# Kernel tuning notes

Hardware: AMD Instinct MI355X
Metric: run time of the kernel (lower is better)

## Reference

```python
import jax, jax.numpy as jnp
import numpy as np

B, N, K, C_IN, D = 4, 2048, 16, 480, 64
EPS = 1e-5


def _c1(x, w, b):
    # 1x1 Conv1d: x (B,C,N), w (O,C) -> (B,O,N)
    return jnp.einsum('oc,bcn->bon', w, x) + b[:, None]


def _c2(x, w, b):
    # 1x1 Conv2d: x (B,C,J,N), w (O,C) -> (B,O,J,N)
    return jnp.einsum('oc,bcjn->bojn', w, x) + b[:, None, None]


def _bn(x, g, b):
    # eval-mode BatchNorm2d with running_mean=0, running_var=1
    return x * (g / jnp.sqrt(1.0 + EPS))[:, None, None] + b[:, None, None]


def _mlp_res(x, w1, b1, w2, b2, ws, bs):
    return _c1(jax.nn.relu(_c1(x, w1, b1)), w2, b2) + _c1(x, ws, bs)


def _group(f, idx):
    # f (B,C,N), idx (B,K,N) int -> out[b,c,j,n] = f[b,c,idx[b,j,n]]  -> (B,C,K,N)
    return jax.vmap(lambda ff, ii: ff[:, ii])(f, idx)


def _knn_idx(xyz):
    # xyz (B,3,N) -> idx (B,K,N), excluding the self point (nearest neighbor)
    pts = xyz.transpose(0, 2, 1)  # (B,N,3)
    sq = jnp.sum(pts * pts, -1)
    d2 = sq[:, :, None] + sq[:, None, :] - 2.0 * jnp.einsum('bnd,bmd->bnm', pts, pts)
    _, idx = jax.lax.top_k(-d2, K + 1)  # (B,N,K+1), nearest first
    return idx.transpose(0, 2, 1)[:, 1:, :]  # drop self -> (B,K,N)


def _forward(idx, feature, xyz, bt1_w, bt1_b, bt2_w, bt2_b, bts_w, bts_b,
             q_w, q_b, k_w, k_b, v_w, v_b,
             fd1_w, fd1_b, fd_g, fd_bb, fd2_w, fd2_b,
             fg1_w, fg1_b, fg_g, fg_bb, fg2_w, fg2_b,
             at_w, at_b, m41_w, m41_b, m42_w, m42_b):
    x = _mlp_res(feature, bt1_w, bt1_b, bt2_w, bt2_b, bts_w, bts_b)  # (B,64,N)
    q = _c1(x, q_w, q_b)
    k = _c1(x, k_w, k_b)
    v = _c1(x, v_w, v_b)

    group_xyz = _group(xyz, idx)                       # (B,3,K,N)
    rel_xyz = xyz[:, :, None, :] - group_xyz           # (B,3,K,N)
    pos_enc = _c2(jax.nn.relu(_bn(_c2(rel_xyz, fd1_w, fd1_b), fd_g, fd_bb)), fd2_w, fd2_b)  # (B,64,K,N)

    k_local = _group(k, idx)                           # (B,64,K,N)
    v_local = _group(v, idx)
    qk_rel = q[:, :, None, :] - k_local
    attn = _c2(jax.nn.relu(_bn(_c2(qk_rel + pos_enc, fg1_w, fg1_b), fg_g, fg_bb)), fg2_w, fg2_b)  # (B,64,K,N)

    attn1 = attn.transpose(0, 1, 3, 2)                 # (B,64,N,K)
    # ConvTranspose2d(64,64,(4,1),(4,1)) with kernel==stride: out[b,o,4n+r,f] = sum_c x[b,c,n,f]*W[c,o,r] + bias[o]
    y = jnp.einsum('bcnf,cor->bonrf', attn1, at_w)
    y = y.reshape(y.shape[0], y.shape[1], -1, y.shape[4]) + at_b[None, :, None, None]  # (B,64,4N,K)
    attn = jax.nn.softmax(y, axis=1)

    value_rel = (v_local + pos_enc).transpose(0, 1, 3, 2)   # (B,64,N,K)
    value = jnp.repeat(value_rel, 4, axis=2)                # nearest upsample (4,1) -> (B,64,4N,K)

    res = jnp.einsum('bmnf,bmnf->bmn', attn, value)         # (B,64,4N)
    identity = jnp.repeat(x, 4, axis=2)                     # nearest upsample x4 -> (B,64,4N)
    res = res + identity
    completion = _c1(jax.nn.relu(_c1(res, m41_w, m41_b)), m42_w, m42_b)  # (B,3,4N)
    return completion, res


def setup_inputs() -> dict:
    key = jax.random.key(0)
    ks = jax.random.split(key, 24)
    i = iter(range(24))

    def w(shape):
        return (jax.random.normal(ks[next(i)], shape, dtype=jnp.float32) * 0.05)

    z = lambda n: jnp.zeros((n,), jnp.float32)
    o = lambda n: jnp.ones((n,), jnp.float32)
    return {
        'feature': jax.random.normal(ks[next(i)], (B, C_IN, N), dtype=jnp.float32),
        'xyz': jax.random.normal(ks[next(i)], (B, 3, N), dtype=jnp.float32),
        'bt1_w': w((D, C_IN)), 'bt1_b': z(D),
        'bt2_w': w((D, D)), 'bt2_b': z(D),
        'bts_w': w((D, C_IN)), 'bts_b': z(D),
        'q_w': w((D, D)), 'q_b': z(D),
        'k_w': w((D, D)), 'k_b': z(D),
        'v_w': w((D, D)), 'v_b': z(D),
        'fd1_w': w((D, 3)), 'fd1_b': z(D), 'fd_g': o(D), 'fd_bb': z(D),
        'fd2_w': w((D, D)), 'fd2_b': z(D),
        'fg1_w': w((4 * D, D)), 'fg1_b': z(4 * D), 'fg_g': o(4 * D), 'fg_bb': z(4 * D),
        'fg2_w': w((D, 4 * D)), 'fg2_b': z(D),
        'at_w': w((D, D, 4)), 'at_b': z(D),
        'm41_w': w((D, D)), 'm41_b': z(D),
        'm42_w': w((3, D)), 'm42_b': z(3),
    }


def reference(feature, xyz, bt1_w, bt1_b, bt2_w, bt2_b, bts_w, bts_b,
              q_w, q_b, k_w, k_b, v_w, v_b,
              fd1_w, fd1_b, fd_g, fd_bb, fd2_w, fd2_b,
              fg1_w, fg1_b, fg_g, fg_bb, fg2_w, fg2_b,
              at_w, at_b, m41_w, m41_b, m42_w, m42_b):
    idx = _knn_idx(xyz)
    return _forward(idx, feature, xyz, bt1_w, bt1_b, bt2_w, bt2_b, bts_w, bts_b,
                    q_w, q_b, k_w, k_b, v_w, v_b,
                    fd1_w, fd1_b, fd_g, fd_bb, fd2_w, fd2_b,
                    fg1_w, fg1_b, fg_g, fg_bb, fg2_w, fg2_b,
                    at_w, at_b, m41_w, m41_b, m42_w, m42_b)
```

## Files before the change

kernel.cpp:

```cpp
#include <hip/hip_runtime.h>

#define B_ 4
#define N_ 2048
#define K_ 16
#define CIN_ 480
#define UPN_ 8192
#define M_ (B_*N_*K_)
#define MX_ (B_*N_)
#define KCAP 448

#define KNN_BLK 2048
#define TR_BLK  1920
#define PREP_BLK 1047

typedef unsigned int u32;
typedef unsigned short u16;
typedef unsigned long long u64;
typedef __attribute__((ext_vector_type(8))) short short8;
typedef __attribute__((ext_vector_type(4))) float f32x4;

#define DEV static __device__ __forceinline__

DEV float b2f(u16 h){ return __uint_as_float(((u32)h)<<16); }
DEV u16 f2b(float f){
  u32 u = __float_as_uint(f);
  u32 r = u + 0x7fffu + ((u>>16)&1u);
  return (u16)(r>>16);
}
DEV u32 cvtpk(float a, float b){
  u32 r; asm("v_cvt_pk_bf16_f32 %0, %1, %2" : "=v"(r) : "v"(a), "v"(b));
  return r;
}
DEV u64 cvtpk4(float a, float b, float c, float d){
  return (u64)cvtpk(a,b) | ((u64)cvtpk(c,d)<<32);
}
DEV bool detect_bf(const void* fg){ return ((((const u32*)fg)[0]) & 0xFFFFu) == 0x3F80u; }
DEV float ld(const void* p, int i, bool bf){
  return bf ? b2f(((const u16*)p)[i]) : ((const float*)p)[i];
}
DEV u64 makekey(float d2, int m){
  u32 bits = __float_as_uint(d2);
  bits = (bits & 0x80000000u) ? ~bits : (bits | 0x80000000u);
  return ((u64)bits<<32) | (u32)m;
}
DEV int swz64 (int row, int colByte){ return row*128 + (colByte ^ ((row&7)<<4)); }
DEV int swz128(int row, int colByte){ return row*256 + (colByte ^ ((row&7)<<4)); }

__global__ __launch_bounds__(256) void setup_kernel(
    const void* __restrict__ feature, const void* __restrict__ xyz,
    const void* __restrict__ bt1_w, const void* __restrict__ bt1_b,
    const void* __restrict__ bt2_w, const void* __restrict__ bt2_b,
    const void* __restrict__ bts_w, const void* __restrict__ bts_b,
    const void* __restrict__ q_w, const void* __restrict__ q_b,
    const void* __restrict__ k_w, const void* __restrict__ k_b,
    const void* __restrict__ v_w, const void* __restrict__ v_b,
    const void* __restrict__ fd1_w, const void* __restrict__ fd1_b,
    const void* __restrict__ fd_g, const void* __restrict__ fd_bb,
    const void* __restrict__ fd2_w, const void* __restrict__ fd2_b,
    const void* __restrict__ fg1_w, const void* __restrict__ fg1_b,
    const void* __restrict__ fg_g, const void* __restrict__ fg_bb,
    const void* __restrict__ fg2_w, const void* __restrict__ fg2_b,
    const void* __restrict__ at_w, const void* __restrict__ at_b,
    const void* __restrict__ m41_w, const void* __restrict__ m41_b,
    const void* __restrict__ m42_w, const void* __restrict__ m42_b,
    float* __restrict__ W, u16* __restrict__ WB,
    u16* __restrict__ fxbT, float* __restrict__ fxyz, int* __restrict__ idx)
{
  __shared__ alignas(16) unsigned char smem[50208];
  int blkid = blockIdx.x;
  bool bf = detect_bf(fd_g);

  if(blkid < KNN_BLK){
    float* px = (float*)smem;
    float* py = px + N_;
    float* pz = py + N_;
    float* sq = pz + N_;
    u64*  sbuf = (u64*)(sq + N_);
    u64*  smin = sbuf + 4*KCAP;
    int*  scnt = (int*)(smin + 256);
    u64*  stau = (u64*)(scnt + 256);
    int bx = blkid & 511;
    int b = blkid >> 9;
    int base = b*3*N_;
    bool w0 = (bx==0);
    for(int i=threadIdx.x;i<N_;i+=256){
      float xx=ld(xyz,base+i,bf), yy=ld(xyz,base+N_+i,bf), zz=ld(xyz,base+2*N_+i,bf);
      px[i]=xx; py[i]=yy; pz[i]=zz; sq[i]=xx*xx+yy*yy+zz*zz;
      if(w0){ fxyz[base+i]=xx; fxyz[base+N_+i]=yy; fxyz[base+2*N_+i]=zz; }
    }
    __syncthreads();
    int w = threadIdx.x>>6, l = threadIdx.x&63;
    int q = bx*4 + w;
    float qx=px[q], qy=py[q], qz=pz[q], qs=sq[q];
    float d2c[32];
    u64 best=~0ull;
    #pragma unroll
    for(int j=0;j<32;j++){
      int m = l*32 + ((j+l)&31);
      float d2 = (qs+sq[m]) - 2.0f*(qx*px[m]+qy*py[m]+qz*pz[m]);
      d2c[j]=d2;
      u64 key = makekey(d2, m);
      best = key<best ? key : best;
    }
    smin[w*64+l]=best;
    __syncthreads();
    {
      int rank=0;
      for(int i=0;i<64;i++) rank += (smin[w*64+i] < best);
      if(rank==16) stau[w] = best;
    }
    __syncthreads();
    u64 tau = stau[w];
    int myc=0;
    #pragma unroll
    for(int j=0;j<32;j++){
      int m = l*32 + ((j+l)&31);
      myc += (makekey(d2c[j], m) <= tau);
    }
    scnt[w*64+l]=myc;
    __syncthreads();
    int off=0, tot=0;
    for(int i=0;i<64;i++){
      int c = scnt[w*64+i];
      tot += c;
      off += (i<l) ? c : 0;
    }
    #pragma unroll
    for(int j=0;j<32;j++){
      int m = l*32 + ((j+l)&31);
      u64 key = makekey(d2c[j], m);
      if(key<=tau && off<KCAP){ sbuf[w*KCAP+off]=key; off++; }
    }
    __syncthreads();
    if(tot>KCAP) tot=KCAP;
    for(int p=l; p<tot; p+=64){
      u64 kk = sbuf[w*KCAP+p];
      int rk=0;
      for(int i=0;i<tot;i++) rk += (sbuf[w*KCAP+i] < kk);
      if(rk>=1 && rk<17) idx[(b*K_+(rk-1))*N_+q] = ((int)(kk & 0xffffffffu)) & (N_-1);
    }
    return;
  }

  if(blkid < KNN_BLK + TR_BLK){
    u16 (*s)[34] = (u16(*)[34])smem;
    int t = blkid - KNN_BLK;
    int ntile = t & 31;  int rest = t >> 5;
    int ctile = rest % 15; int b = rest / 15;
    int tx = threadIdx.x & 31, ty = threadIdx.x >> 5;
    u64 base = (u64)b*CIN_*N_;
    #pragma unroll
    for(int r=0;r<4;r++){
      int c = ctile*32 + ty + r*8;
      u64 i = base + (u64)c*N_ + ntile*64 + tx*2;
      u32 v;
      if(bf) v = *(const u32*)((const u16*)feature + i);
      else {
        float a0=((const float*)feature)[i], a1=((const float*)feature)[i+1];
        v = (u32)f2b(a0) | ((u32)f2b(a1)<<16);
      }
      s[tx*2  ][ty + r*8] = (u16)v;
      s[tx*2+1][ty + r*8] = (u16)(v>>16);
    }
    __syncthreads();
    #pragma unroll
    for(int r=0;r<4;r++){
      int i2 = r*256 + threadIdx.x;
      int nrow = i2 >> 4, cp = i2 & 15;
      u32 v = *(const u32*)&s[nrow][cp*2];
      int n = ntile*64 + nrow;
      *(u32*)(fxbT + (u64)b*N_*CIN_ + (u64)n*CIN_ + ctile*32 + cp*2) = v;
    }
    return;
  }

  int t = (blkid - (KNN_BLK + TR_BLK))*256 + threadIdx.x;
  const float inv = 0.9999950000374997f;
  if(t < 30720) return; t -= 30720;
  if(t < 30720) return; t -= 30720;
  if(t < 4096) return; t -= 4096;
  if(t < 4096) return; t -= 4096;
  if(t < 4096) return; t -= 4096;
  if(t < 4096) return; t -= 4096;
  if(t < 256){
    int o=t>>2, j=t&3; float s = ld(fd_g,o,bf)*inv;
    W[77824+t] = (j<3) ? s*ld(fd1_w,o*3+j,bf) : (s*ld(fd1_b,o,bf) + ld(fd_bb,o,bf));
    return;
  } t -= 256;
  if(t < 4096) return; t -= 4096;
  if(t < 16384) return; t -= 16384;
  if(t < 256){ float s=ld(fg_g,t,bf)*inv; W[98560+t] = s*ld(fg1_b,t,bf) + ld(fg_bb,t,bf); return; } t -= 256;
  if(t < 16384) return; t -= 16384;
  if(t < 16384) return; t -= 16384;
  if(t < 4096){ int m=t>>6, o=t&63; W[131584+t] = ld(m41_w,o*64+m,bf); return; } t -= 4096;
  if(t < 192){ W[135680+t] = ld(m42_w,t,bf); return; } t -= 192;
  if(t < 64){ W[135872+t] = ld(bt1_b,t,bf); return; } t -= 64;
  if(t < 64){ W[135936+t] = ld(bts_b,t,bf); return; } t -= 64;
  if(t < 64){ W[136000+t] = ld(bt2_b,t,bf); return; } t -= 64;
  if(t < 64){ W[136064+t] = ld(q_b,t,bf); return; } t -= 64;
  if(t < 64){ W[136128+t] = ld(k_b,t,bf); return; } t -= 64;
  if(t < 64){ W[136192+t] = ld(v_b,t,bf); return; } t -= 64;
  if(t < 64){ W[136256+t] = ld(fd2_b,t,bf); return; } t -= 64;
  if(t < 64){ W[136320+t] = ld(fg2_b,t,bf); return; } t -= 64;
  if(t < 64){ W[136384+t] = ld(at_b,t,bf); return; } t -= 64;
  if(t < 64){ W[136448+t] = ld(m41_b,t,bf); return; } t -= 64;
  if(t < 3){ W[136512+t] = ld(m42_b,t,bf); return; } t -= 3;
  if(t < 16384){ int o=t>>6; float s=ld(fg_g,o,bf)*inv; WB[t] = f2b(s*ld(fg1_w,t,bf)); return; } t -= 16384;
  if(t < 16384){ WB[16384+t] = f2b(ld(fg2_w,t,bf)); return; } t -= 16384;
  if(t < 16384){ int j=t>>6, c=t&63;
                 WB[32768+t] = f2b(ld(at_w,(c*64+(j&63))*4+(j>>6),bf)); return; } t -= 16384;
  if(t < 256){ W[136576+t] = ld(at_b,t&63,bf); return; } t -= 256;
  if(t < 4096){ WB[49152+t] = f2b(ld(fd2_w,t,bf)); return; } t -= 4096;
  if(t < 30720){ WB[53248+t] = f2b(ld(bt1_w,t,bf)); return; } t -= 30720;
  if(t < 30720){ WB[83968+t] = f2b(ld(bts_w,t,bf)); return; } t -= 30720;
  if(t < 4096){ WB[114688+t] = f2b(ld(bt2_w,t,bf)); return; } t -= 4096;
  if(t < 4096){ WB[118784+t] = f2b(ld(q_w,t,bf)); return; } t -= 4096;
  if(t < 4096){ WB[122880+t] = f2b(ld(k_w,t,bf)); return; } t -= 4096;
  if(t < 4096){ WB[126976+t] = f2b(ld(v_w,t,bf)); return; }
}

__global__ __launch_bounds__(256) void gemm480_mfma(const u16* __restrict__ A,
    const u16* __restrict__ Wt, const float* __restrict__ bias,
    u16* __restrict__ hout, float* __restrict__ xsout)
{
  int tid=threadIdx.x, w=tid>>6, lane=tid&63;
  int rbase=(blockIdx.x*4+w)*16;
  int cbase=blockIdx.y*64;
  int lr=lane&15, lk=(lane>>4)*8;
  f32x4 acc[4];
  #pragma unroll
  for(int j=0;j<4;j++) acc[j]=(f32x4){0.f,0.f,0.f,0.f};
  for(int kc=0;kc<CIN_;kc+=32){
    short8 a = *(const short8*)(A + (u64)(rbase+lr)*CIN_ + kc + lk);
    #pragma unroll
    for(int tj=0;tj<4;tj++){
      short8 bb = *(const short8*)(Wt + (u64)(cbase+tj*16+lr)*CIN_ + kc + lk);
      acc[tj] = __builtin_amdgcn_mfma_f32_16x16x32_bf16(a, bb, acc[tj], 0,0,0);
    }
  }
  int rq=(lane>>4)*4;
  #pragma unroll
  for(int tj=0;tj<4;tj++){
    int col = cbase + tj*16 + lr;
    float bv = bias[col];
    #pragma unroll
    for(int reg=0;reg<4;reg++){
      u64 row = rbase + rq + reg;
      float vv = acc[tj][reg] + bv;
      if(blockIdx.y==0) hout[row*64 + col] = f2b(fmaxf(vv,0.f));
      else              xsout[row*64 + (col-64)] = vv;
    }
  }
}

__global__ __launch_bounds__(256) void xqkv_mfma(const u16* __restrict__ A,
    const u16* __restrict__ Wbt2, const float* __restrict__ bbt2,
    const float* __restrict__ xs,
    const u16* __restrict__ Wqkv, const float* __restrict__ bqkv,
    float* __restrict__ x, float* __restrict__ qkvout)
{
  __shared__ alignas(16) unsigned char lds[8192];
  int tid=threadIdx.x, w=tid>>6, lane=tid&63;
  int lr=lane&15, lk=(lane>>4)*8, rq=(lane>>4)*4;
  unsigned char* Lw = lds + w*2048;
  u64 rbase=(u64)(blockIdx.x*4+w)*16;

  {
    f32x4 ax[4];
    #pragma unroll
    for(int i=0;i<4;i++) ax[i]=(f32x4){0.f,0.f,0.f,0.f};
    #pragma unroll
    for(int kc=0;kc<64;kc+=32){
      short8 hf = *(const short8*)(A + (rbase+lr)*64 + kc + lk);
      #pragma unroll
      for(int t=0;t<4;t++){
        short8 wf = *(const short8*)(Wbt2 + (u64)(t*16+lr)*64 + kc + lk);
        ax[t] = __builtin_amdgcn_mfma_f32_16x16x32_bf16(wf, hf, ax[t], 0,0,0);
      }
    }
    #pragma unroll
    for(int t=0;t<4;t++){
      f32x4 bb = *(const f32x4*)(bbt2 + t*16 + rq);
      f32x4 sv = *(const f32x4*)(xs + (rbase+lr)*64 + t*16 + rq);
      f32x4 xv;
      #pragma unroll
      for(int reg=0;reg<4;reg++) xv[reg] = ax[t][reg] + bb[reg] + sv[reg];
      *(f32x4*)(x + (rbase+lr)*64 + t*16 + rq) = xv;
      *(u64*)(Lw + swz64(lr, (t*16+rq)*2)) = cvtpk4(xv[0],xv[1],xv[2],xv[3]);
    }
  }
  __syncthreads();
  #pragma unroll
  for(int g=0;g<3;g++){
    f32x4 aq[4];
    #pragma unroll
    for(int i=0;i<4;i++) aq[i]=(f32x4){0.f,0.f,0.f,0.f};
    #pragma unroll
    for(int kc=0;kc<64;kc+=32){
      short8 hf = *(const short8*)(Lw + swz64(lr, (kc+lk)*2));
      #pragma unroll
      for(int t=0;t<4;t++){
        short8 wf = *(const short8*)(Wqkv + (u64)(g*64+t*16+lr)*64 + kc + lk);
        aq[t] = __builtin_amdgcn_mfma_f32_16x16x32_bf16(wf, hf, aq[t], 0,0,0);
      }
    }
    #pragma unroll
    for(int t=0;t<4;t++){
      f32x4 bq = *(const f32x4*)(bqkv + g*64 + t*16 + rq);
      f32x4 ov;
      #pragma unroll
      for(int reg=0;reg<4;reg++) ov[reg] = aq[t][reg] + bq[reg];
      *(f32x4*)(qkvout + (rbase+lr)*192 + g*64 + t*16 + rq) = ov;
    }
  }
}

__global__ __launch_bounds__(256) void fused_chain(
    const int* __restrict__ idx, const float* __restrict__ fxyz,
    const float* __restrict__ qkv, const float* __restrict__ x,
    const float* __restrict__ fd1f,
    const u16* __restrict__ Wfd2, const float* __restrict__ bfd2,
    const u16* __restrict__ Wfg1, const float* __restrict__ bfg1,
    const u16* __restrict__ Wfg2, const float* __restrict__ bfg2,
    const u16* __restrict__ Wat,  const float* __restrict__ bat,
    const float* __restrict__ cm41T, const float* __restrict__ cm41b,
    const float* __restrict__ cm42f, const float* __restrict__ cm42b,
    const void* __restrict__ det, void* __restrict__ out)
{
  __shared__ alignas(16) unsigned char lds[32768];
  int tid = threadIdx.x;
  int w = tid>>6, lane = tid&63;
  int lr = lane&15, lk = (lane>>4)*8, rq = (lane>>4)*4;

  int erow = tid>>2, ecg = tid&3;
  int el = erow>>4, ef = erow&15;
  int bn_e = blockIdx.x*4 + el;
  int b_e = bn_e>>11, n_e = bn_e&(N_-1);
  int jn = idx[(b_e*K_+ef)*N_ + n_e] & (N_-1);

  {
    const float* xb = fxyz + (u64)b_e*3*N_;
    float rx = xb[n_e]      - xb[jn];
    float ry = xb[N_+n_e]   - xb[N_+jn];
    float rz = xb[2*N_+n_e] - xb[2*N_+jn];
    #pragma unroll
    for(int gg=0; gg<4; gg++){
      float tv[4];
      #pragma unroll
      for(int j=0;j<4;j++){
        f32x4 wv = *(const f32x4*)(fd1f + ((ecg*4+gg)*4+j)*4);
        tv[j] = fmaxf(wv[0]*rx + wv[1]*ry + wv[2]*rz + wv[3], 0.f);
      }
      *(u64*)(lds + swz64(erow, (ecg*4+gg)*8)) = cvtpk4(tv[0],tv[1],tv[2],tv[3]);
    }
  }
  __syncthreads();

  {
    f32x4 acc[4];
    #pragma unroll
    for(int i=0;i<4;i++) acc[i]=(f32x4){0.f,0.f,0.f,0.f};
    #pragma unroll
    for(int kc=0;kc<64;kc+=32){
      short8 wf = *(const short8*)(Wfd2 + (u64)(w*16+lr)*64 + kc + lk);
      #pragma unroll
      for(int ti=0;ti<4;ti++){
        short8 tf = *(const short8*)(lds + swz64(ti*16+lr, (kc+lk)*2));
        acc[ti] = __builtin_amdgcn_mfma_f32_16x16x32_bf16(wf, tf, acc[ti], 0,0,0);
      }
    }
    f32x4 b4 = *(const f32x4*)(bfd2 + w*16 + rq);
    #pragma unroll
    for(int ti=0;ti<4;ti++)
      *(u64*)(lds + 8192 + swz64(ti*16+lr, (w*16+rq)*2)) =
        cvtpk4(acc[ti][0]+b4[0], acc[ti][1]+b4[1], acc[ti][2]+b4[2], acc[ti][3]+b4[3]);
  }
  __syncthreads();

  {
    int mg = ecg*16;
    const float* qrow = qkv + (u64)(b_e*N_+n_e)*192 + mg;
    const float* krow = qkv + (u64)(b_e*N_+jn)*192 + 64 + mg;
    const float* vrow = qkv + (u64)(b_e*N_+jn)*192 + 128 + mg;
    #pragma unroll
    for(int g2=0; g2<4; g2++){
      f32x4 qv = *(const f32x4*)(qrow + g2*4);
      f32x4 kv = *(const f32x4*)(krow + g2*4);
      f32x4 vv = *(const f32x4*)(vrow + g2*4);
      int cb = (mg + g2*4)*2;
      u64 pw = *(const u64*)(lds + 8192 + swz64(erow, cb));
      float p0=b2f((u16)pw), p1=b2f((u16)(pw>>16)), p2=b2f((u16)(pw>>32)), p3=b2f((u16)(pw>>48));
      *(u64*)(lds + swz64(erow, cb)) =
        cvtpk4(qv[0]-kv[0]+p0, qv[1]-kv[1]+p1, qv[2]-kv[2]+p2, qv[3]-kv[3]+p3);
      *(u64*)(lds + 8192 + swz64(erow, cb)) =
        cvtpk4(vv[0]+p0, vv[1]+p1, vv[2]+p2, vv[3]+p3);
    }
  }
  __syncthreads();

  float vreg[16];
  #pragma unroll
  for(int f2=0; f2<16; f2++)
    vreg[f2] = b2f(*(const u16*)(lds + 8192 + swz64(w*16+f2, lane*2)));

  f32x4 gacc[4];
  #pragma unroll
  for(int i=0;i<4;i++) gacc[i]=(f32x4){0.f,0.f,0.f,0.f};
  #pragma unroll
  for(int half=0; half<2; half++){
    {
      f32x4 hacc[2][4];
      #pragma unroll
      for(int i=0;i<2;i++)
        #pragma unroll
        for(int j=0;j<4;j++) hacc[i][j]=(f32x4){0.f,0.f,0.f,0.f};
      #pragma unroll
      for(int kc=0;kc<64;kc+=32){
        short8 wf[2], af[4];
        #pragma unroll
        for(int ti=0;ti<2;ti++)
          wf[ti] = *(const short8*)(Wfg1 + (u64)(half*128 + w*32 + ti*16 + lr)*64 + kc + lk);
        #pragma unroll
        for(int tj=0;tj<4;tj++)
          af[tj] = *(const short8*)(lds + swz64(tj*16+lr, (kc+lk)*2));
        #pragma unroll
        for(int ti=0;ti<2;ti++)
          #pragma unroll
          for(int tj=0;tj<4;tj++)
            hacc[ti][tj] = __builtin_amdgcn_mfma_f32_16x16x32_bf16(wf[ti], af[tj], hacc[ti][tj], 0,0,0);
      }
      #pragma unroll
      for(int ti=0;ti<2;ti++){
        f32x4 b4 = *(const f32x4*)(bfg1 + half*128 + w*32 + ti*16 + rq);
        #pragma unroll
        for(int tj=0;tj<4;tj++){
          int row = tj*16 + lr;
          *(u64*)(lds + 16384 + swz128(row, (w*32+ti*16+rq)*2)) =
            cvtpk4(fmaxf(hacc[ti][tj][0]+b4[0],0.f), fmaxf(hacc[ti][tj][1]+b4[1],0.f),
                   fmaxf(hacc[ti][tj][2]+b4[2],0.f), fmaxf(hacc[ti][tj][3]+b4[3],0.f));
        }
      }
    }
    __syncthreads();
    #pragma unroll
    for(int kc=0;kc<128;kc+=32){
      short8 wf = *(const short8*)(Wfg2 + (u64)(w*16+lr)*256 + half*128 + kc + lk);
      #pragma unroll
      for(int tj=0;tj<4;tj++){
        short8 hf = *(const short8*)(lds + 16384 + swz128(tj*16+lr, (kc+lk)*2));
        gacc[tj] = __builtin_amdgcn_mfma_f32_16x16x32_bf16(wf, hf, gacc[tj], 0,0,0);
      }
    }
    __syncthreads();
  }

  {
    f32x4 b4 = *(const f32x4*)(bfg2 + w*16 + rq);
    #pragma unroll
    for(int tj=0;tj<4;tj++)
      *(u64*)(lds + swz64(tj*16+lr, (w*16+rq)*2)) =
        cvtpk4(gacc[tj][0]+b4[0], gacc[tj][1]+b4[1], gacc[tj][2]+b4[2], gacc[tj][3]+b4[3]);
  }
  __syncthreads();

  float aout[4];
  int srow = tid>>2, sub = tid&3;
  #pragma unroll
  for(int r=0;r<4;r++){
    {
      f32x4 acc[4];
      #pragma unroll
      for(int i=0;i<4;i++) acc[i]=(f32x4){0.f,0.f,0.f,0.f};
      #pragma unroll
      for(int kc=0;kc<64;kc+=32){
        short8 wf = *(const short8*)(Wat + (u64)(r*64 + w*16 + lr)*64 + kc + lk);
        #pragma unroll
        for(int tj=0;tj<4;tj++){
          short8 gf = *(const short8*)(lds + swz64(tj*16+lr, (kc+lk)*2));
          acc[tj] = __builtin_amdgcn_mfma_f32_16x16x32_bf16(wf, gf, acc[tj], 0,0,0);
        }
      }
      f32x4 b4 = *(const f32x4*)(bat + r*64 + w*16 + rq);
      #pragma unroll
      for(int tj=0;tj<4;tj++)
        *(u64*)(lds + 16384 + swz64(tj*16+lr, (w*16+rq)*2)) =
          cvtpk4(acc[tj][0]+b4[0], acc[tj][1]+b4[1], acc[tj][2]+b4[2], acc[tj][3]+b4[3]);
    }
    __syncthreads();
    {
      float yv[16];
      uint4 pk0 = *(const uint4*)(lds + 16384 + swz64(srow, sub*32));
      uint4 pk1 = *(const uint4*)(lds + 16384 + swz64(srow, sub*32 + 16));
      yv[0]=__uint_as_float(pk0.x<<16); yv[1]=__uint_as_float(pk0.x&0xffff0000u);
      yv[2]=__uint_as_float(pk0.y<<16); yv[3]=__uint_as_float(pk0.y&0xffff0000u);
      yv[4]=__uint_as_float(pk0.z<<16); yv[5]=__uint_as_float(pk0.z&0xffff0000u);
      yv[6]=__uint_as_float(pk0.w<<16); yv[7]=__uint_as_float(pk0.w&0xffff0000u);
      yv[8]=__uint_as_float(pk1.x<<16); yv[9]=__uint_as_float(pk1.x&0xffff0000u);
      yv[10]=__uint_as_float(pk1.y<<16); yv[11]=__uint_as_float(pk1.y&0xffff0000u);
      yv[12]=__uint_as_float(pk1.z<<16); yv[13]=__uint_as_float(pk1.z&0xffff0000u);
      yv[14]=__uint_as_float(pk1.w<<16); yv[15]=__uint_as_float(pk1.w&0xffff0000u);
      float mx = yv[0];
      #pragma unroll
      for(int m=1;m<16;m++) mx = fmaxf(mx, yv[m]);
      mx = fmaxf(mx, __shfl_xor(mx, 1));
      mx = fmaxf(mx, __shfl_xor(mx, 2));
      float sm = 0.f;
      #pragma unroll
      for(int m=0;m<16;m++){ float e = __expf(yv[m]-mx); yv[m]=e; sm+=e; }
      sm += __shfl_xor(sm, 1);
      sm += __shfl_xor(sm, 2);
      float rinv = 1.0f/sm;
      uint4 o0, o1;
      o0.x = cvtpk(yv[0]*rinv, yv[1]*rinv);  o0.y = cvtpk(yv[2]*rinv, yv[3]*rinv);
      o0.z = cvtpk(yv[4]*rinv, yv[5]*rinv);  o0.w = cvtpk(yv[6]*rinv, yv[7]*rinv);
      o1.x = cvtpk(yv[8]*rinv, yv[9]*rinv);  o1.y = cvtpk(yv[10]*rinv, yv[11]*rinv);
      o1.z = cvtpk(yv[12]*rinv, yv[13]*rinv); o1.w = cvtpk(yv[14]*rinv, yv[15]*rinv);
      *(uint4*)(lds + 8192 + swz64(srow, sub*32))      = o0;
      *(uint4*)(lds + 8192 + swz64(srow, sub*32 + 16)) = o1;
    }
    __syncthreads();
    {
      float a = 0.f;
      #pragma unroll
      for(int f2=0; f2<16; f2++)
        a += b2f(*(const u16*)(lds + 8192 + swz64(w*16+f2, lane*2))) * vreg[f2];
      aout[r] = a;
    }
  }

  int bn = blockIdx.x*4 + w;
  int b = bn>>11, n = bn&(N_-1);
  float xv = x[(u64)bn*64 + lane];
  u64 off = 98304 + ((u64)(b*64+lane))*UPN_ + (u64)n*4;
  bool bf = detect_bf(det);
  float rv0, rv1, rv2, rv3;
  if(bf){
    u64 pk = cvtpk4(aout[0]+xv, aout[1]+xv, aout[2]+xv, aout[3]+xv);
    *(u64*)((u16*)out + off) = pk;
    rv0 = b2f((u16)pk); rv1 = b2f((u16)(pk>>16));
    rv2 = b2f((u16)(pk>>32)); rv3 = b2f((u16)(pk>>48));
  } else {
    f32x4 pk = {aout[0]+xv, aout[1]+xv, aout[2]+xv, aout[3]+xv};
    *(f32x4*)((float*)out + off) = pk;
    rv0 = pk[0]; rv1 = pk[1]; rv2 = pk[2]; rv3 = pk[3];
  }
  float* L = (float*)(lds + w*1024);
  *(f32x4*)(L + lane*4) = (f32x4){rv0, rv1, rv2, rv3};

  __syncthreads();
  {
    f32x4* dst = (f32x4*)(lds + 8192);
    const f32x4* src = (const f32x4*)cm41T;
    #pragma unroll
    for(int i=0;i<4;i++) dst[tid + i*256] = src[tid + i*256];
  }
  __syncthreads();

  const float* Lw41 = (const float*)(lds + 8192);
  f32x4 acc4;
  {
    float bo = cm41b[lane];
    acc4 = (f32x4){bo, bo, bo, bo};
    #pragma unroll 8
    for(int c=0;c<64;c++){
      float wv = Lw41[c*64 + lane];
      f32x4 rr = *(const f32x4*)(L + c*4);
      acc4[0] += wv*rr[0]; acc4[1] += wv*rr[1];
      acc4[2] += wv*rr[2]; acc4[3] += wv*rr[3];
    }
  }
  f32x4 h2 = {fmaxf(acc4[0],0.f), fmaxf(acc4[1],0.f),
              fmaxf(acc4[2],0.f), fmaxf(acc4[3],0.f)};
  *(f32x4*)(L + lane*4) = h2;
  if(lane < 12){
    int coord = lane>>2, r2 = lane&3;
    float sum = cm42b[coord];
    #pragma unroll 4
    for(int o=0;o<64;o++)
      sum += cm42f[coord*64+o] * L[o*4 + r2];
    u64 base = (u64)b*3*UPN_ + (u64)coord*UPN_ + (u64)n*4 + r2;
    if(bf) ((u16*)out)[base] = f2b(sum);
    else   ((float*)out)[base] = sum;
  }
}

extern "C" void kernel_launch(void* const* d_in, const int* in_sizes, int n_in,
                              void* d_out, int out_size, void* d_ws, size_t ws_size,
                              hipStream_t stream)
{
  (void)in_sizes; (void)n_in; (void)out_size; (void)ws_size;
  const void* feature=d_in[0];
  const void* xyz   =d_in[1];
  const void* bt1_w =d_in[2];  const void* bt1_b=d_in[3];
  const void* bt2_w =d_in[4];  const void* bt2_b=d_in[5];
  const void* bts_w =d_in[6];  const void* bts_b=d_in[7];
  const void* q_w   =d_in[8];  const void* q_b =d_in[9];
  const void* k_w   =d_in[10]; const void* k_b =d_in[11];
  const void* v_w   =d_in[12]; const void* v_b =d_in[13];
  const void* fd1_w =d_in[14]; const void* fd1_b=d_in[15];
  const void* fd_g  =d_in[16]; const void* fd_bb=d_in[17];
  const void* fd2_w =d_in[18]; const void* fd2_b=d_in[19];
  const void* fg1_w =d_in[20]; const void* fg1_b=d_in[21];
  const void* fg_g  =d_in[22]; const void* fg_bb=d_in[23];
  const void* fg2_w =d_in[24]; const void* fg2_b=d_in[25];
  const void* at_w  =d_in[26]; const void* at_b =d_in[27];
  const void* m41_w =d_in[28]; const void* m41_b=d_in[29];
  const void* m42_w =d_in[30]; const void* m42_b=d_in[31];

  char* ws=(char*)d_ws;
  float* W   =(float*)(ws);
  u16*  WB   =(u16*)  (ws + 589824);
  int*  idx  =(int*)  (ws + 851968);
  float* x   =(float*)(ws + 1376256);
  float* qkv =(float*)(ws + 3473408);
  u16*  h    =(u16*)  (ws + 9764864);
  float* xs  =(float*)(ws + 10813440);
  u16*  fxbT =(u16*)  (ws + 114622464);
  float* fxyz=(float*)(ws + 122486784);

  const float* W_fd1f = W+77824;
  const float* W_fg1fb= W+98560;
  const float* W_m41T = W+131584;
  const float* W_m42  = W+135680;
  const float* Wb_g480= W+135872;
  const float* Wb_bt2 = W+136000;
  const float* Wb_qkv = W+136064;
  const float* Wb_fd2 = W+136256;
  const float* Wb_fg2 = W+136320;
  const float* Wb_m41 = W+136448;
  const float* Wb_m42 = W+136512;
  const float* W_atb256 = W+136576;
  const u16* WB_fg1  = WB;
  const u16* WB_fg2  = WB+16384;
  const u16* WB_at   = WB+32768;
  const u16* WB_fd2  = WB+49152;
  const u16* WB_g480 = WB+53248;
  const u16* WB_bt2  = WB+114688;
  const u16* WB_qkv  = WB+118784;

  setup_kernel<<<KNN_BLK+TR_BLK+PREP_BLK,256,0,stream>>>(feature, xyz,
      bt1_w,bt1_b,bt2_w,bt2_b,bts_w,bts_b,q_w,q_b,k_w,k_b,
      v_w,v_b,fd1_w,fd1_b,fd_g,fd_bb,fd2_w,fd2_b,fg1_w,fg1_b,fg_g,fg_bb,fg2_w,fg2_b,
      at_w,at_b,m41_w,m41_b,m42_w,m42_b,W,WB,fxbT,fxyz,idx);
  gemm480_mfma<<<dim3(MX_/64,2),256,0,stream>>>(fxbT, WB_g480, Wb_g480, h, xs);
  xqkv_mfma<<<MX_/64,256,0,stream>>>(h, WB_bt2, Wb_bt2, xs, WB_qkv, Wb_qkv, x, qkv);
  fused_chain<<<B_*N_/4,256,0,stream>>>(idx, fxyz, qkv, x, W_fd1f,
      WB_fd2, Wb_fd2, WB_fg1, W_fg1fb, WB_fg2, Wb_fg2, WB_at, W_atb256,
      W_m41T, Wb_m41, W_m42, Wb_m42, fd_g, d_out);
}
```

Baseline: 245.3 us.

## Fuse 480-channel input GEMM into the x/qkv prefix kernel

Merges the gemm480 kernel, which wrote the relu hidden activations h and the shortcut xs to global memory, into the following x/qkv kernel. The hidden tile now goes through LDS, and the shortcut accumulator stays in registers, so the intermediate global round trip and one kernel launch are removed. In exchange the grid halves (one block computes both output halves), each wave holds twice the accumulators, and LDS use doubles, which may reduce parallelism for the 480-deep GEMM.

```diff
diff --git a/kernel.cpp b/kernel.cpp
--- a/kernel.cpp
+++ b/kernel.cpp
@@ -219,51 +219,43 @@
   if(t < 4096){ WB[126976+t] = f2b(ld(v_w,t,bf)); return; }
 }
 
-__global__ __launch_bounds__(256) void gemm480_mfma(const u16* __restrict__ A,
-    const u16* __restrict__ Wt, const float* __restrict__ bias,
-    u16* __restrict__ hout, float* __restrict__ xsout)
-{
-  int tid=threadIdx.x, w=tid>>6, lane=tid&63;
-  int rbase=(blockIdx.x*4+w)*16;
-  int cbase=blockIdx.y*64;
-  int lr=lane&15, lk=(lane>>4)*8;
-  f32x4 acc[4];
-  #pragma unroll
-  for(int j=0;j<4;j++) acc[j]=(f32x4){0.f,0.f,0.f,0.f};
-  for(int kc=0;kc<CIN_;kc+=32){
-    short8 a = *(const short8*)(A + (u64)(rbase+lr)*CIN_ + kc + lk);
-    #pragma unroll
-    for(int tj=0;tj<4;tj++){
-      short8 bb = *(const short8*)(Wt + (u64)(cbase+tj*16+lr)*CIN_ + kc + lk);
-      acc[tj] = __builtin_amdgcn_mfma_f32_16x16x32_bf16(a, bb, acc[tj], 0,0,0);
-    }
-  }
-  int rq=(lane>>4)*4;
-  #pragma unroll
-  for(int tj=0;tj<4;tj++){
-    int col = cbase + tj*16 + lr;
-    float bv = bias[col];
-    #pragma unroll
-    for(int reg=0;reg<4;reg++){
-      u64 row = rbase + rq + reg;
-      float vv = acc[tj][reg] + bv;
-      if(blockIdx.y==0) hout[row*64 + col] = f2b(fmaxf(vv,0.f));
-      else              xsout[row*64 + (col-64)] = vv;
-    }
-  }
-}
-
-__global__ __launch_bounds__(256) void xqkv_mfma(const u16* __restrict__ A,
+__global__ __launch_bounds__(256) void prefix_mfma(const u16* __restrict__ A,
+    const u16* __restrict__ Wg, const float* __restrict__ bg,
     const u16* __restrict__ Wbt2, const float* __restrict__ bbt2,
-    const float* __restrict__ xs,
     const u16* __restrict__ Wqkv, const float* __restrict__ bqkv,
     float* __restrict__ x, float* __restrict__ qkvout)
 {
-  __shared__ alignas(16) unsigned char lds[8192];
+  __shared__ alignas(16) unsigned char lds[16384];
   int tid=threadIdx.x, w=tid>>6, lane=tid&63;
   int lr=lane&15, lk=(lane>>4)*8, rq=(lane>>4)*4;
-  unsigned char* Lw = lds + w*2048;
+  unsigned char* Lh = lds + w*4096;
+  unsigned char* Lx = Lh + 2048;
   u64 rbase=(u64)(blockIdx.x*4+w)*16;
+
+  f32x4 ah[4], as4[4];
+  #pragma unroll
+  for(int i=0;i<4;i++){ ah[i]=(f32x4){0.f,0.f,0.f,0.f}; as4[i]=(f32x4){0.f,0.f,0.f,0.f}; }
+  for(int kc=0;kc<CIN_;kc+=32){
+    short8 af = *(const short8*)(A + (rbase+lr)*CIN_ + kc + lk);
+    #pragma unroll
+    for(int t=0;t<4;t++){
+      short8 wh = *(const short8*)(Wg + (u64)(t*16+lr)*CIN_ + kc + lk);
+      ah[t] = __builtin_amdgcn_mfma_f32_16x16x32_bf16(wh, af, ah[t], 0,0,0);
+    }
+    #pragma unroll
+    for(int t=0;t<4;t++){
+      short8 ws = *(const short8*)(Wg + (u64)(64+t*16+lr)*CIN_ + kc + lk);
+      as4[t] = __builtin_amdgcn_mfma_f32_16x16x32_bf16(ws, af, as4[t], 0,0,0);
+    }
+  }
+  #pragma unroll
+  for(int t=0;t<4;t++){
+    f32x4 b4 = *(const f32x4*)(bg + t*16 + rq);
+    *(u64*)(Lh + swz64(lr, (t*16+rq)*2)) =
+      cvtpk4(fmaxf(ah[t][0]+b4[0],0.f), fmaxf(ah[t][1]+b4[1],0.f),
+             fmaxf(ah[t][2]+b4[2],0.f), fmaxf(ah[t][3]+b4[3],0.f));
+  }
+  __syncthreads();
 
   {
     f32x4 ax[4];
@@ -271,7 +263,7 @@
     for(int i=0;i<4;i++) ax[i]=(f32x4){0.f,0.f,0.f,0.f};
     #pragma unroll
     for(int kc=0;kc<64;kc+=32){
-      short8 hf = *(const short8*)(A + (rbase+lr)*64 + kc + lk);
+      short8 hf = *(const short8*)(Lh + swz64(lr, (kc+lk)*2));
       #pragma unroll
       for(int t=0;t<4;t++){
         short8 wf = *(const short8*)(Wbt2 + (u64)(t*16+lr)*64 + kc + lk);
@@ -281,15 +273,17 @@
     #pragma unroll
     for(int t=0;t<4;t++){
       f32x4 bb = *(const f32x4*)(bbt2 + t*16 + rq);
-      f32x4 sv = *(const f32x4*)(xs + (rbase+lr)*64 + t*16 + rq);
+      f32x4 bs = *(const f32x4*)(bg + 64 + t*16 + rq);
       f32x4 xv;
       #pragma unroll
-      for(int reg=0;reg<4;reg++) xv[reg] = ax[t][reg] + bb[reg] + sv[reg];
+      for(int reg=0;reg<4;reg++)
+        xv[reg] = ax[t][reg] + bb[reg] + (as4[t][reg] + bs[reg]);
       *(f32x4*)(x + (rbase+lr)*64 + t*16 + rq) = xv;
-      *(u64*)(Lw + swz64(lr, (t*16+rq)*2)) = cvtpk4(xv[0],xv[1],xv[2],xv[3]);
-    }
-  }
-  __syncthreads();
+      *(u64*)(Lx + swz64(lr, (t*16+rq)*2)) = cvtpk4(xv[0],xv[1],xv[2],xv[3]);
+    }
+  }
+  __syncthreads();
+
   #pragma unroll
   for(int g=0;g<3;g++){
     f32x4 aq[4];
@@ -297,7 +291,7 @@
     for(int i=0;i<4;i++) aq[i]=(f32x4){0.f,0.f,0.f,0.f};
     #pragma unroll
     for(int kc=0;kc<64;kc+=32){
-      short8 hf = *(const short8*)(Lw + swz64(lr, (kc+lk)*2));
+      short8 hf = *(const short8*)(Lx + swz64(lr, (kc+lk)*2));
       #pragma unroll
       for(int t=0;t<4;t++){
         short8 wf = *(const short8*)(Wqkv + (u64)(g*64+t*16+lr)*64 + kc + lk);
@@ -613,8 +607,6 @@
   int*  idx  =(int*)  (ws + 851968);
   float* x   =(float*)(ws + 1376256);
   float* qkv =(float*)(ws + 3473408);
-  u16*  h    =(u16*)  (ws + 9764864);
-  float* xs  =(float*)(ws + 10813440);
   u16*  fxbT =(u16*)  (ws + 114622464);
   float* fxyz=(float*)(ws + 122486784);
 
@@ -642,8 +634,8 @@
       bt1_w,bt1_b,bt2_w,bt2_b,bts_w,bts_b,q_w,q_b,k_w,k_b,
       v_w,v_b,fd1_w,fd1_b,fd_g,fd_bb,fd2_w,fd2_b,fg1_w,fg1_b,fg_g,fg_bb,fg2_w,fg2_b,
       at_w,at_b,m41_w,m41_b,m42_w,m42_b,W,WB,fxbT,fxyz,idx);
-  gemm480_mfma<<<dim3(MX_/64,2),256,0,stream>>>(fxbT, WB_g480, Wb_g480, h, xs);
-  xqkv_mfma<<<MX_/64,256,0,stream>>>(h, WB_bt2, Wb_bt2, xs, WB_qkv, Wb_qkv, x, qkv);
+  prefix_mfma<<<MX_/64,256,0,stream>>>(fxbT, WB_g480, Wb_g480,
+      WB_bt2, Wb_bt2, WB_qkv, Wb_qkv, x, qkv);
   fused_chain<<<B_*N_/4,256,0,stream>>>(idx, fxyz, qkv, x, W_fd1f,
       WB_fd2, Wb_fd2, WB_fg1, W_fg1fb, WB_fg2, Wb_fg2, WB_at, W_atb256,
       W_m41T, Wb_m41, W_m42, Wb_m42, fd_g, d_out);
```

Measured after the change: 271.6 us. +10.7%, slower.
